# Performance work log

Measured on AMD Instinct MI355X. Metric: run time of the kernel, lower is better.

Reference implementation:

```python
import jax, jax.numpy as jnp
import numpy as np

EPS = 1e-5
ROPE_BASE = 10000.0

def rms_norm(x, w):
    return x * jax.lax.rsqrt(jnp.mean(x * x, axis=-1, keepdims=True) + EPS) * w

def rope_cos_sin(positions, head_dim):
    inv_freq = 1.0 / (ROPE_BASE ** (jnp.arange(0, head_dim, 2, dtype=jnp.float32) / head_dim))
    ang = positions.astype(jnp.float32)[:, None] * inv_freq[None, :]          # [L, hd/2]
    emb = jnp.concatenate([ang, ang], axis=-1)                                # [L, hd]
    return jnp.cos(emb), jnp.sin(emb)

def rotate_half(x):
    d = x.shape[-1] // 2
    return jnp.concatenate([-x[..., d:], x[..., :d]], axis=-1)

def apply_rope(x, cos, sin):
    # x: [B,H,L,hd]; cos/sin: [L,hd]
    return x * cos[None, None] + rotate_half(x) * sin[None, None]

def setup_inputs() -> dict:
    key = jax.random.key(0)
    ks = jax.random.split(key, 12)
    B, S, D = 1, 2048, 2048
    H, KVH, HD = 16, 8, 128
    FF, CACHE = 5632, 2048
    s = 0.02
    return {
        "hidden_states": jax.random.normal(ks[0], (B, S, D), jnp.float32),
        "k_cache": jax.random.normal(ks[1], (B, H, CACHE, HD), jnp.float32),
        "v_cache": jax.random.normal(ks[2], (B, H, CACHE, HD), jnp.float32),
        "q_w": jax.random.normal(ks[3], (H * HD, D), jnp.float32) * s,
        "k_w": jax.random.normal(ks[4], (KVH * HD, D), jnp.float32) * s,
        "v_w": jax.random.normal(ks[5], (KVH * HD, D), jnp.float32) * s,
        "o_w": jax.random.normal(ks[6], (D, H * HD), jnp.float32) * s,
        "gate_w": jax.random.normal(ks[7], (FF, D), jnp.float32) * s,
        "up_w": jax.random.normal(ks[8], (FF, D), jnp.float32) * s,
        "down_w": jax.random.normal(ks[9], (D, FF), jnp.float32) * s,
        "ln1_w": jnp.ones((D,), jnp.float32),
        "ln2_w": jnp.ones((D,), jnp.float32),
        "chunk_size": 512,
    }

def reference(hidden_states, k_cache, v_cache, q_w, k_w, v_w, o_w,
              gate_w, up_w, down_w, ln1_w, ln2_w, chunk_size):
    B, S, D = hidden_states.shape
    H = k_cache.shape[1]
    HD = k_cache.shape[-1]
    KVH = k_w.shape[0] // HD
    group = H // KVH
    prefix = k_cache.shape[2]

    # --- input RMSNorm ---
    residual = hidden_states
    h = rms_norm(hidden_states, ln1_w)

    # --- QKV projections (GQA) ---
    q = (h @ q_w.T).reshape(B, S, H, HD).transpose(0, 2, 1, 3)                # [B,H,S,hd]
    k = (h @ k_w.T).reshape(B, S, KVH, HD).transpose(0, 2, 1, 3)              # [B,KVH,S,hd]
    v = (h @ v_w.T).reshape(B, S, KVH, HD).transpose(0, 2, 1, 3)
    k = jnp.repeat(k, group, axis=1)                                          # repeat_kv -> [B,H,S,hd]
    v = jnp.repeat(v, group, axis=1)

    # --- KV-cache concat along seq ---
    keys = jnp.concatenate([k_cache, k], axis=2)                              # [B,H,P+S,hd]
    vals = jnp.concatenate([v_cache, v], axis=2)
    kv_len = prefix + S

    # --- inline RoPE: keys at 0..kv_len-1, queries at prefix..kv_len-1 ---
    cos_k, sin_k = rope_cos_sin(jnp.arange(kv_len), HD)
    q = apply_rope(q, cos_k[prefix:], sin_k[prefix:])
    keys = apply_rope(keys, cos_k, sin_k)

    # --- hybrid chunked attention mask ---
    # query i (local) sees: full cache prefix + causal positions within its own chunk
    i = jnp.arange(S)
    j = jnp.arange(kv_len)
    local_j = j - prefix
    prefix_vis = (j[None, :] < prefix)
    same_chunk = (i[:, None] // chunk_size) == (local_j[None, :] // chunk_size)
    causal = local_j[None, :] <= i[:, None]
    mask = prefix_vis | (same_chunk & causal)                                 # [S, kv_len]

    scores = jnp.einsum("bhqd,bhkd->bhqk", q, keys) / jnp.sqrt(jnp.float32(HD))
    scores = jnp.where(mask[None, None], scores, jnp.finfo(scores.dtype).min)
    probs = jax.nn.softmax(scores, axis=-1)
    attn = jnp.einsum("bhqk,bhkd->bhqd", probs, vals)                         # [B,H,S,hd]
    attn = attn.transpose(0, 2, 1, 3).reshape(B, S, H * HD) @ o_w.T

    h = residual + attn

    # --- SwiGLU MLP ---
    residual = h
    h = rms_norm(h, ln2_w)
    h = (jax.nn.silu(h @ gate_w.T) * (h @ up_w.T)) @ down_w.T
    return residual + h
```

## Files before the change

kernel.cpp:

```cpp
#include <hip/hip_runtime.h>


#define S_LEN   2048
#define D_MODEL 2048
#define NH      16
#define KVHEADS 8
#define HDIM    128
#define FFDIM   5632
#define PREFIX  2048
#define KVLEN   4096
#define SM_L2E  0.12751744f
#define MCONST  16.0f
#define LN10K_64 0.14391156831212787f

using bf16x8 = __attribute__((ext_vector_type(8))) short;
using f32x4  = __attribute__((ext_vector_type(4))) float;

__device__ __forceinline__ unsigned f2bf_u(float f) {
  unsigned u = __float_as_uint(f);
  return (u + 0x7fffu + ((u >> 16) & 1u)) >> 16;
}
__device__ __forceinline__ unsigned short f2bf(float f) { return (unsigned short)f2bf_u(f); }
__device__ __forceinline__ float bf2f(unsigned short u) {
  return __uint_as_float((unsigned)u << 16);
}
__device__ __forceinline__ unsigned pack2(float a, float b) {
  return f2bf_u(a) | (f2bf_u(b) << 16);
}
__device__ __forceinline__ uint2 pack4(float4 v) {
  uint2 r;
  r.x = pack2(v.x, v.y);
  r.y = pack2(v.z, v.w);
  return r;
}
__device__ __forceinline__ f32x4 mfma16(bf16x8 a, bf16x8 b, f32x4 c) {
  return __builtin_amdgcn_mfma_f32_16x16x32_bf16(a, b, c, 0, 0, 0);
}
__device__ __forceinline__ void gl2lds16(const unsigned short* g, unsigned short* l) {
  __builtin_amdgcn_global_load_lds(
      (__attribute__((address_space(1))) void*)(unsigned short*)g,
      (__attribute__((address_space(3))) void*)l, 16, 0, 0);
}

__device__ __forceinline__ void conv_body(const float* __restrict__ src,
                                          unsigned short* __restrict__ dst,
                                          int bseg, int tid) {
  size_t i = (size_t)bseg * 256 + tid;
  const float4* s4 = (const float4*)src;
  float4 a = s4[2 * i], b = s4[2 * i + 1];
  uint2 lo = pack4(a), hi = pack4(b);
  ((uint4*)dst)[i] = make_uint4(lo.x, lo.y, hi.x, hi.y);
}
__global__ __launch_bounds__(256) void convw_k(const float* __restrict__ src,
                                               unsigned short* __restrict__ dst) {
  conv_body(src, dst, blockIdx.x, threadIdx.x);
}
__global__ __launch_bounds__(256) void conv3_k(const float* __restrict__ q,
                                               const float* __restrict__ k,
                                               const float* __restrict__ v,
                                               unsigned short* __restrict__ dst) {
  int b = blockIdx.x;
  if (b < 2048)      conv_body(q, dst, b, threadIdx.x);
  else if (b < 3072) conv_body(k, dst + (size_t)2048 * 2048, b - 2048, threadIdx.x);
  else               conv_body(v, dst + (size_t)3072 * 2048, b - 3072, threadIdx.x);
}
__global__ __launch_bounds__(256) void conv2_k(const float* __restrict__ g,
                                               const float* __restrict__ u,
                                               unsigned short* __restrict__ wg,
                                               unsigned short* __restrict__ wu) {
  int b = blockIdx.x;
  if (b < 5632) conv_body(g, wg, b, threadIdx.x);
  else          conv_body(u, wu, b - 5632, threadIdx.x);
}

template <bool INBF>
__global__ __launch_bounds__(256) void rmsnorm_k(const void* __restrict__ xin,
                                                 const float* __restrict__ w,
                                                 unsigned short* __restrict__ out) {
  const int row = blockIdx.x, tid = threadIdx.x;
  float v[8];
  if constexpr (INBF) {
    const unsigned short* xr = (const unsigned short*)xin + (size_t)row * D_MODEL;
    uint4 u = ((const uint4*)xr)[tid];
    v[0] = bf2f((unsigned short)(u.x & 0xffff)); v[1] = bf2f((unsigned short)(u.x >> 16));
    v[2] = bf2f((unsigned short)(u.y & 0xffff)); v[3] = bf2f((unsigned short)(u.y >> 16));
    v[4] = bf2f((unsigned short)(u.z & 0xffff)); v[5] = bf2f((unsigned short)(u.z >> 16));
    v[6] = bf2f((unsigned short)(u.w & 0xffff)); v[7] = bf2f((unsigned short)(u.w >> 16));
  } else {
    const float4* xr = (const float4*)((const float*)xin + (size_t)row * D_MODEL);
    float4 a = xr[2 * tid], b = xr[2 * tid + 1];
    v[0] = a.x; v[1] = a.y; v[2] = a.z; v[3] = a.w;
    v[4] = b.x; v[5] = b.y; v[6] = b.z; v[7] = b.w;
  }
  float ss = 0.f;
#pragma unroll
  for (int i = 0; i < 8; i++) ss += v[i] * v[i];
#pragma unroll
  for (int off = 1; off < 64; off <<= 1) ss += __shfl_xor(ss, off);
  __shared__ float red[4];
  if ((tid & 63) == 0) red[tid >> 6] = ss;
  __syncthreads();
  const float sc = rsqrtf((red[0] + red[1] + red[2] + red[3]) * (1.0f / D_MODEL) + 1e-5f);
  const float4* w4 = (const float4*)w;
  float4 wa = w4[2 * tid], wb = w4[2 * tid + 1];
  float4 oa = make_float4(v[0]*sc*wa.x, v[1]*sc*wa.y, v[2]*sc*wa.z, v[3]*sc*wa.w);
  float4 ob = make_float4(v[4]*sc*wb.x, v[5]*sc*wb.y, v[6]*sc*wb.z, v[7]*sc*wb.w);
  uint2 lo = pack4(oa), hi = pack4(ob);
  ((uint4*)(out + (size_t)row * D_MODEL))[tid] = make_uint4(lo.x, lo.y, hi.x, hi.y);
}

template <int BN, int EPI>
__global__ __launch_bounds__(256) void gemm_bf(const unsigned short* __restrict__ A,
                                               const unsigned short* __restrict__ B,
                                               const void* __restrict__ res,
                                               void* __restrict__ C,
                                               int M, int N, int K) {
  constexpr int NI = BN / 32;
  __shared__ __align__(16) unsigned short lA[128 * 32];
  __shared__ __align__(16) unsigned short lB[BN * 32];
  const int tid = threadIdx.x, lane = tid & 63, wave = tid >> 6;
  const int r16 = lane & 15, q4 = lane >> 4;
  const int wm = wave >> 1, wn = wave & 1;
  const int nwg = gridDim.x * gridDim.y;
  const int flat = blockIdx.y * gridDim.x + blockIdx.x;
  const int swz = (flat & 7) * (nwg >> 3) + (flat >> 3);
  const int m0 = (swz % gridDim.x) * 128, n0 = (swz / gridDim.x) * BN;

  const int lr = lane >> 2;
  const int lc = (lane & 3) * 8;
  const unsigned short* gA0 = A + (size_t)(m0 + wave * 16 + lr) * K + lc;
  const unsigned short* gA1 = A + (size_t)(m0 + 64 + wave * 16 + lr) * K + lc;
  unsigned short* lA0 = lA + (wave * 16) * 32;
  unsigned short* lA1 = lA + (64 + wave * 16) * 32;
  const unsigned short* gB0 = B + (size_t)(n0 + wave * 16 + lr) * K + lc;
  const unsigned short* gB1 = B + (size_t)(n0 + 64 + wave * 16 + lr) * K + lc;
  unsigned short* lB0 = lB + (wave * 16) * 32;
  unsigned short* lB1 = lB + (64 + wave * 16) * 32;

  f32x4 acc[4][NI];
#pragma unroll
  for (int i = 0; i < 4; i++)
#pragma unroll
    for (int j = 0; j < NI; j++) acc[i][j] = f32x4{0.f, 0.f, 0.f, 0.f};

  for (int k0 = 0; k0 < K; k0 += 32) {
    gl2lds16(gA0, lA0);
    gl2lds16(gA1, lA1);
    gl2lds16(gB0, lB0);
    if constexpr (BN == 128) gl2lds16(gB1, lB1);
    gA0 += 32; gA1 += 32; gB0 += 32;
    if constexpr (BN == 128) gB1 += 32;
    __syncthreads();
    bf16x8 af[4], bfr[NI];
#pragma unroll
    for (int mi = 0; mi < 4; mi++)
      af[mi] = *(const bf16x8*)&lA[(wm * 64 + mi * 16 + r16) * 32 + q4 * 8];
#pragma unroll
    for (int ni = 0; ni < NI; ni++)
      bfr[ni] = *(const bf16x8*)&lB[(wn * (BN / 2) + ni * 16 + r16) * 32 + q4 * 8];
#pragma unroll
    for (int mi = 0; mi < 4; mi++)
#pragma unroll
      for (int ni = 0; ni < NI; ni++)
        acc[mi][ni] = mfma16(af[mi], bfr[ni], acc[mi][ni]);
    __syncthreads();
  }
#pragma unroll
  for (int mi = 0; mi < 4; mi++)
#pragma unroll
    for (int ni = 0; ni < NI; ni++) {
      int col = n0 + wn * (BN / 2) + ni * 16 + r16;
#pragma unroll
      for (int rr = 0; rr < 4; rr++) {
        int row = m0 + wm * 64 + mi * 16 + q4 * 4 + rr;
        size_t idx = (size_t)row * N + col;
        float v = acc[mi][ni][rr];
        if constexpr (EPI == 0) {
          ((unsigned short*)C)[idx] = f2bf(v);
        } else if constexpr (EPI == 1) {
          ((unsigned short*)C)[idx] = f2bf(v + ((const float*)res)[idx]);
        } else {
          ((float*)C)[idx] = v + bf2f(((const unsigned short*)res)[idx]);
        }
      }
    }
}

__global__ __launch_bounds__(256) void gemm_gateup(const unsigned short* __restrict__ A,
                                                   const unsigned short* __restrict__ Bg,
                                                   const unsigned short* __restrict__ Bu,
                                                   unsigned short* __restrict__ act) {
  __shared__ __align__(16) unsigned short lA[128 * 32];
  __shared__ __align__(16) unsigned short lG[64 * 32];
  __shared__ __align__(16) unsigned short lU[64 * 32];
  const int tid = threadIdx.x, lane = tid & 63, wave = tid >> 6;
  const int r16 = lane & 15, q4 = lane >> 4;
  const int wm = wave >> 1, wn = wave & 1;
  const int nwg = gridDim.x * gridDim.y;
  const int flat = blockIdx.y * gridDim.x + blockIdx.x;
  const int swz = (flat & 7) * (nwg >> 3) + (flat >> 3);
  const int m0 = (swz % gridDim.x) * 128, n0 = (swz / gridDim.x) * 64;
  const int K = D_MODEL;

  const int lr = lane >> 2, lc = (lane & 3) * 8;
  const unsigned short* gA0 = A + (size_t)(m0 + wave * 16 + lr) * K + lc;
  const unsigned short* gA1 = A + (size_t)(m0 + 64 + wave * 16 + lr) * K + lc;
  unsigned short* lA0 = lA + (wave * 16) * 32;
  unsigned short* lA1 = lA + (64 + wave * 16) * 32;
  const unsigned short* gG0 = Bg + (size_t)(n0 + wave * 16 + lr) * K + lc;
  const unsigned short* gU0 = Bu + (size_t)(n0 + wave * 16 + lr) * K + lc;
  unsigned short* lG0 = lG + (wave * 16) * 32;
  unsigned short* lU0 = lU + (wave * 16) * 32;

  f32x4 ag[4][2], au[4][2];
#pragma unroll
  for (int i = 0; i < 4; i++)
#pragma unroll
    for (int j = 0; j < 2; j++) { ag[i][j] = f32x4{0.f,0.f,0.f,0.f}; au[i][j] = f32x4{0.f,0.f,0.f,0.f}; }

  for (int k0 = 0; k0 < K; k0 += 32) {
    gl2lds16(gA0, lA0);
    gl2lds16(gA1, lA1);
    gl2lds16(gG0, lG0);
    gl2lds16(gU0, lU0);
    gA0 += 32; gA1 += 32; gG0 += 32; gU0 += 32;
    __syncthreads();
    bf16x8 af[4], bg2[2], bu2[2];
#pragma unroll
    for (int mi = 0; mi < 4; mi++)
      af[mi] = *(const bf16x8*)&lA[(wm * 64 + mi * 16 + r16) * 32 + q4 * 8];
#pragma unroll
    for (int ni = 0; ni < 2; ni++) {
      int r = (wn * 32 + ni * 16 + r16) * 32 + q4 * 8;
      bg2[ni] = *(const bf16x8*)&lG[r];
      bu2[ni] = *(const bf16x8*)&lU[r];
    }
#pragma unroll
    for (int mi = 0; mi < 4; mi++)
#pragma unroll
      for (int ni = 0; ni < 2; ni++) {
        ag[mi][ni] = mfma16(af[mi], bg2[ni], ag[mi][ni]);
        au[mi][ni] = mfma16(af[mi], bu2[ni], au[mi][ni]);
      }
    __syncthreads();
  }
#pragma unroll
  for (int mi = 0; mi < 4; mi++)
#pragma unroll
    for (int ni = 0; ni < 2; ni++) {
      int col = n0 + wn * 32 + ni * 16 + r16;
#pragma unroll
      for (int rr = 0; rr < 4; rr++) {
        int row = m0 + wm * 64 + mi * 16 + q4 * 4 + rr;
        float g = ag[mi][ni][rr], u = au[mi][ni][rr];
        float sil = g / (1.0f + __expf(-g));
        act[(size_t)row * FFDIM + col] = f2bf(sil * u);
      }
    }
}

__global__ __launch_bounds__(256) void rope_k_k(const float* __restrict__ k_cache,
                                                const unsigned short* __restrict__ qkv,
                                                unsigned short* __restrict__ keys_bf) {
  int idx = blockIdx.x * 256 + threadIdx.x;
  int d = idx & 127, j = (idx >> 7) & 4095, h = idx >> 19;
  int dd = d & 63;
  float inv = __expf(-(float)dd * LN10K_64);
  float ang = (float)j * inv;
  float c = cosf(ang), sn = sinf(ang);
  float x, xr;
  if (j < PREFIX) {
    const float* row = k_cache + ((size_t)h * PREFIX + j) * HDIM;
    x = row[d];
    xr = (d < 64) ? -row[d + 64] : row[d - 64];
  } else {
    const unsigned short* row = qkv + (size_t)(j - PREFIX) * 4096 + 2048 + (h >> 1) * HDIM;
    x = bf2f(row[d]);
    xr = (d < 64) ? -bf2f(row[d + 64]) : bf2f(row[d - 64]);
  }
  keys_bf[idx] = f2bf(x * c + xr * sn);
}

__global__ __launch_bounds__(256) void vtrans_k(const float* __restrict__ v_cache,
                                                const unsigned short* __restrict__ qkv,
                                                unsigned short* __restrict__ vals_t) {
  __shared__ float tile[32][33];
  const int h = blockIdx.z, j0 = blockIdx.x * 32, d0 = blockIdx.y * 32;
  const int t = threadIdx.x;
#pragma unroll
  for (int i = 0; i < 4; i++) {
    int e = i * 256 + t;
    int jj = e >> 5, dd = e & 31;
    float v;
    if (j0 < PREFIX)
      v = v_cache[((size_t)h * PREFIX + j0 + jj) * HDIM + d0 + dd];
    else
      v = bf2f(qkv[(size_t)(j0 - PREFIX + jj) * 4096 + 3072 + (h >> 1) * HDIM + d0 + dd]);
    tile[jj][dd] = v;
  }
  __syncthreads();
#pragma unroll
  for (int i = 0; i < 4; i++) {
    int e = i * 256 + t;
    int dd = e >> 5, jj = e & 31;
    vals_t[((size_t)h * HDIM + d0 + dd) * KVLEN + j0 + jj] = f2bf(tile[jj][dd]);
  }
}

__global__ __launch_bounds__(256) void attn_k(const unsigned short* __restrict__ qkv,
                                              const unsigned short* __restrict__ keys,
                                              const unsigned short* __restrict__ valst,
                                              const int* __restrict__ chunkp,
                                              unsigned short* __restrict__ pO,
                                              float* __restrict__ pl) {
  __shared__ __align__(16) unsigned short lK[64 * 128];
  __shared__ __align__(16) unsigned short lV[128 * 64];
  __shared__ __align__(16) unsigned short lP[4][16 * 64];
  const int flat = blockIdx.x;
  const int xcd = flat & 7, ii = flat >> 3;
  const int p = ii >> 5;
  const int seg = p >> 1;
  const int h = xcd * 2 + (p & 1);
  const int q0 = (ii & 31) * 64;
  const int tid = threadIdx.x, wave = tid >> 6, lane = tid & 63;
  const int r16 = lane & 15, q4 = lane >> 4;
  const int chunk = chunkp[0];
  const int sw = (r16 & 7) << 4;

  const int qrow = q0 + wave * 16 + r16;
  const unsigned short* qr = qkv + (size_t)qrow * 4096 + h * HDIM;
  float qx[4][8];
#pragma unroll
  for (int ks = 0; ks < 4; ks++) {
    bf16x8 raw = *(const bf16x8*)(qr + ks * 32 + q4 * 8);
#pragma unroll
    for (int j = 0; j < 8; j++) qx[ks][j] = bf2f((unsigned short)raw[j]);
  }
  const float pos = (float)(PREFIX + qrow);
  bf16x8 qf[4];
#pragma unroll
  for (int ks = 0; ks < 4; ks++)
#pragma unroll
    for (int j = 0; j < 8; j++) {
      int d = ks * 32 + q4 * 8 + j;
      float inv = __expf(-(float)(d & 63) * LN10K_64);
      float ang = pos * inv;
      float c = cosf(ang), sn = sinf(ang);
      float other = qx[ks ^ 2][j];
      float rot = (ks < 2) ? -other : other;
      qf[ks][j] = (short)f2bf(qx[ks][j] * c + rot * sn);
    }

  float lrow[4] = {0.f, 0.f, 0.f, 0.f};
  f32x4 oacc[8];
#pragma unroll
  for (int ni = 0; ni < 8; ni++) oacc[ni] = f32x4{0.f, 0.f, 0.f, 0.f};

  const int irow_base = q0 + wave * 16 + q4 * 4;
  const unsigned short* Kh = keys + (size_t)h * KVLEN * HDIM;
  const unsigned short* Vh = valst + (size_t)h * HDIM * KVLEN;

  const int krow = wave * 4 + (lane >> 4);
  const unsigned short* kSrc = Kh + (size_t)(krow * 4) * HDIM
                               + (((lane & 15) ^ (krow & 7)) * 8);
  unsigned short* kDst = lK + (wave * 4) * 128;
  const int vrow = wave * 8 + (lane >> 3);
  const unsigned short* vSrc = Vh + (size_t)vrow * KVLEN
                               + (((lane & 7) ^ ((lane >> 3) & 7)) * 8);
  unsigned short* vDst = lV + (wave * 8) * 64;

  int kt0, ktN;
  if (seg == 0)      { kt0 = 0;    ktN = 1024; }
  else if (seg == 1) { kt0 = 1024; ktN = 2048; }
  else { int cs = (q0 / chunk) * chunk; kt0 = PREFIX + cs; ktN = PREFIX + q0 + 64; }

  for (int kt = kt0; kt < ktN; kt += 64) {
    const bool domask = (seg == 2) && (kt - PREFIX + 64 > q0);
#pragma unroll
    for (int i = 0; i < 4; i++)
      gl2lds16(kSrc + (size_t)(kt + i) * HDIM, kDst + i * 16 * 128);
#pragma unroll
    for (int i = 0; i < 4; i++)
      gl2lds16(vSrc + (size_t)i * 32 * KVLEN + kt, vDst + i * 32 * 64);
    __syncthreads();
    f32x4 s[4];
#pragma unroll
    for (int j = 0; j < 4; j++) s[j] = f32x4{0.f, 0.f, 0.f, 0.f};
#pragma unroll
    for (int ks = 0; ks < 4; ks++)
#pragma unroll
      for (int j = 0; j < 4; j++) {
        bf16x8 kf = *(const bf16x8*)((const char*)lK + (j * 16 + r16) * 256
                                     + ((ks * 64 + q4 * 16) ^ sw));
        s[j] = mfma16(qf[ks], kf, s[j]);
      }
    const int klb = kt - PREFIX + r16 * 4;
#pragma unroll
    for (int rr = 0; rr < 4; rr++) {
      float e0 = fmaf(s[0][rr], SM_L2E, -MCONST);
      float e1 = fmaf(s[1][rr], SM_L2E, -MCONST);
      float e2 = fmaf(s[2][rr], SM_L2E, -MCONST);
      float e3 = fmaf(s[3][rr], SM_L2E, -MCONST);
      if (domask) {
        int irow = irow_base + rr;
        if (klb     > irow) e0 = -1e30f;
        if (klb + 1 > irow) e1 = -1e30f;
        if (klb + 2 > irow) e2 = -1e30f;
        if (klb + 3 > irow) e3 = -1e30f;
      }
      float p0 = exp2f(e0), p1 = exp2f(e1), p2 = exp2f(e2), p3 = exp2f(e3);
      lrow[rr] += (p0 + p1) + (p2 + p3);
      uint2 pk = make_uint2(pack2(p0, p1), pack2(p2, p3));
      int qrw = q4 * 4 + rr;
      *(uint2*)((char*)lP[wave] + qrw * 128 + ((r16 * 8) ^ ((qrw & 7) << 4))) = pk;
    }
    bf16x8 pf0 = *(const bf16x8*)((const char*)lP[wave] + r16 * 128
                                  + ((q4 * 16) ^ sw));
    bf16x8 pf1 = *(const bf16x8*)((const char*)lP[wave] + r16 * 128
                                  + ((64 + q4 * 16) ^ sw));
#pragma unroll
    for (int ni = 0; ni < 8; ni++) {
      bf16x8 v0 = *(const bf16x8*)((const char*)lV + (ni * 16 + r16) * 128
                                   + ((q4 * 16) ^ sw));
      oacc[ni] = mfma16(pf0, v0, oacc[ni]);
      bf16x8 v1 = *(const bf16x8*)((const char*)lV + (ni * 16 + r16) * 128
                                   + ((64 + q4 * 16) ^ sw));
      oacc[ni] = mfma16(pf1, v1, oacc[ni]);
    }
    __syncthreads();
  }

#pragma unroll
  for (int rr = 0; rr < 4; rr++) {
    lrow[rr] += __shfl_xor(lrow[rr], 1);
    lrow[rr] += __shfl_xor(lrow[rr], 2);
    lrow[rr] += __shfl_xor(lrow[rr], 4);
    lrow[rr] += __shfl_xor(lrow[rr], 8);
  }
  const size_t base = (size_t)(seg * NH + h) * S_LEN;
#pragma unroll
  for (int ni = 0; ni < 8; ni++)
#pragma unroll
    for (int rr = 0; rr < 4; rr++)
      pO[(base + irow_base + rr) * HDIM + ni * 16 + r16] = f2bf(oacc[ni][rr]);
  if (r16 == 0) {
#pragma unroll
    for (int rr = 0; rr < 4; rr++) pl[base + irow_base + rr] = lrow[rr];
  }
}

__global__ __launch_bounds__(256) void attn_combine(const unsigned short* __restrict__ pO,
                                                    const float* __restrict__ pl,
                                                    unsigned short* __restrict__ out) {
  int idx = blockIdx.x * 256 + threadIdx.x;
  int d = idx & 127, hq = idx >> 7;
  const int R = NH * S_LEN;
  float L = pl[hq] + pl[hq + R] + pl[hq + 2 * R];
  float o = bf2f(pO[(size_t)hq * HDIM + d])
          + bf2f(pO[(size_t)(hq + R) * HDIM + d])
          + bf2f(pO[(size_t)(hq + 2 * R) * HDIM + d]);
  int h = hq >> 11, q = hq & 2047;
  out[(size_t)q * D_MODEL + h * HDIM + d] = f2bf(o / L);
}

extern "C" void kernel_launch(void* const* d_in, const int* in_sizes, int n_in,
                              void* d_out, int out_size, void* d_ws, size_t ws_size,
                              hipStream_t stream) {
  (void)in_sizes; (void)n_in; (void)out_size;
  const float* hidden  = (const float*)d_in[0];
  const float* k_cache = (const float*)d_in[1];
  const float* v_cache = (const float*)d_in[2];
  const float* q_w     = (const float*)d_in[3];
  const float* k_w     = (const float*)d_in[4];
  const float* v_w     = (const float*)d_in[5];
  const float* o_w     = (const float*)d_in[6];
  const float* gate_w  = (const float*)d_in[7];
  const float* up_w    = (const float*)d_in[8];
  const float* down_w  = (const float*)d_in[9];
  const float* ln1     = (const float*)d_in[10];
  const float* ln2     = (const float*)d_in[11];
  const int*   chunkp  = (const int*)d_in[12];

  if (ws_size < 92274688) return;
  char* ws = (char*)d_ws;
  const size_t MB = 1048576;
  unsigned short* qkvpre = (unsigned short*)(ws + 0 * MB);
  unsigned short* keysbf = (unsigned short*)(ws + 16 * MB);
  unsigned short* valst  = (unsigned short*)(ws + 32 * MB);
  unsigned short* pO     = (unsigned short*)(ws + 48 * MB);
  float*          pl     = (float*)(ws + 88 * MB - 393216);
  unsigned short* WQKV   = (unsigned short*)(ws + 72 * MB);
  unsigned short* hn     = (unsigned short*)(ws + 48 * MB);
  unsigned short* attnbf = (unsigned short*)(ws + 72 * MB);
  unsigned short* WO     = (unsigned short*)(ws + 80 * MB);
  unsigned short* h2     = (unsigned short*)(ws + 48 * MB);
  unsigned short* h2n    = (unsigned short*)(ws + 56 * MB);
  unsigned short* WG     = (unsigned short*)(ws + 0 * MB);
  unsigned short* WU     = (unsigned short*)(ws + 22 * MB);
  unsigned short* act    = (unsigned short*)(ws + 64 * MB);
  unsigned short* WD     = (unsigned short*)(ws + 0 * MB);
  float* out = (float*)d_out;

  rmsnorm_k<false><<<S_LEN, 256, 0, stream>>>(hidden, ln1, hn);
  conv3_k<<<4096, 256, 0, stream>>>(q_w, k_w, v_w, WQKV);
  gemm_bf<128, 0><<<dim3(16, 32), 256, 0, stream>>>(hn, WQKV, nullptr, qkvpre,
                                                    S_LEN, 4096, D_MODEL);
  rope_k_k<<<(NH * KVLEN * HDIM) / 256, 256, 0, stream>>>(k_cache, qkvpre, keysbf);
  vtrans_k<<<dim3(KVLEN / 32, HDIM / 32, NH), 256, 0, stream>>>(v_cache, qkvpre, valst);
  attn_k<<<1536, 256, 0, stream>>>(qkvpre, keysbf, valst, chunkp, pO, pl);
  attn_combine<<<(NH * S_LEN * HDIM) / 256, 256, 0, stream>>>(pO, pl, attnbf);
  convw_k<<<2048, 256, 0, stream>>>(o_w, WO);
  gemm_bf<64, 1><<<dim3(16, 32), 256, 0, stream>>>(attnbf, WO, hidden, h2,
                                                   S_LEN, D_MODEL, D_MODEL);
  rmsnorm_k<true><<<S_LEN, 256, 0, stream>>>(h2, ln2, h2n);
  conv2_k<<<11264, 256, 0, stream>>>(gate_w, up_w, WG, WU);
  gemm_gateup<<<dim3(16, FFDIM / 64), 256, 0, stream>>>(h2n, WG, WU, act);
  convw_k<<<5632, 256, 0, stream>>>(down_w, WD);
  gemm_bf<64, 2><<<dim3(16, 32), 256, 0, stream>>>(act, WD, h2, out,
                                                   S_LEN, D_MODEL, FFDIM);
}
```

Baseline: 697.4 us.

## Enlarge gate/up GEMM N-tile and attention query tile to 128 rows

The gate/up GEMM now computes a 128x128 output tile per block instead of 128x64, so each staged A tile is reused across twice as many columns and the grid is halved. The attention kernel now gives each wave two 16-row query tiles (128 queries per block), so every K/V tile loaded into shared memory serves twice as many queries, with half the blocks. Both changes aim to cut global-to-LDS traffic per FLOP. In exchange they roughly double accumulator registers, which may lower occupancy, and the attention grid shrinks to 768 blocks. For the chunk-local segment the causal range also becomes coarser.

```diff
diff --git a/kernel.cpp b/kernel.cpp
--- a/kernel.cpp
+++ b/kernel.cpp
@@ -191,15 +191,15 @@
                                                    const unsigned short* __restrict__ Bu,
                                                    unsigned short* __restrict__ act) {
   __shared__ __align__(16) unsigned short lA[128 * 32];
-  __shared__ __align__(16) unsigned short lG[64 * 32];
-  __shared__ __align__(16) unsigned short lU[64 * 32];
+  __shared__ __align__(16) unsigned short lG[128 * 32];
+  __shared__ __align__(16) unsigned short lU[128 * 32];
   const int tid = threadIdx.x, lane = tid & 63, wave = tid >> 6;
   const int r16 = lane & 15, q4 = lane >> 4;
   const int wm = wave >> 1, wn = wave & 1;
   const int nwg = gridDim.x * gridDim.y;
   const int flat = blockIdx.y * gridDim.x + blockIdx.x;
   const int swz = (flat & 7) * (nwg >> 3) + (flat >> 3);
-  const int m0 = (swz % gridDim.x) * 128, n0 = (swz / gridDim.x) * 64;
+  const int m0 = (swz % gridDim.x) * 128, n0 = (swz / gridDim.x) * 128;
   const int K = D_MODEL;
 
   const int lr = lane >> 2, lc = (lane & 3) * 8;
@@ -208,37 +208,43 @@
   unsigned short* lA0 = lA + (wave * 16) * 32;
   unsigned short* lA1 = lA + (64 + wave * 16) * 32;
   const unsigned short* gG0 = Bg + (size_t)(n0 + wave * 16 + lr) * K + lc;
+  const unsigned short* gG1 = Bg + (size_t)(n0 + 64 + wave * 16 + lr) * K + lc;
   const unsigned short* gU0 = Bu + (size_t)(n0 + wave * 16 + lr) * K + lc;
+  const unsigned short* gU1 = Bu + (size_t)(n0 + 64 + wave * 16 + lr) * K + lc;
   unsigned short* lG0 = lG + (wave * 16) * 32;
+  unsigned short* lG1 = lG + (64 + wave * 16) * 32;
   unsigned short* lU0 = lU + (wave * 16) * 32;
-
-  f32x4 ag[4][2], au[4][2];
+  unsigned short* lU1 = lU + (64 + wave * 16) * 32;
+
+  f32x4 ag[4][4], au[4][4];
 #pragma unroll
   for (int i = 0; i < 4; i++)
 #pragma unroll
-    for (int j = 0; j < 2; j++) { ag[i][j] = f32x4{0.f,0.f,0.f,0.f}; au[i][j] = f32x4{0.f,0.f,0.f,0.f}; }
+    for (int j = 0; j < 4; j++) { ag[i][j] = f32x4{0.f,0.f,0.f,0.f}; au[i][j] = f32x4{0.f,0.f,0.f,0.f}; }
 
   for (int k0 = 0; k0 < K; k0 += 32) {
     gl2lds16(gA0, lA0);
     gl2lds16(gA1, lA1);
     gl2lds16(gG0, lG0);
+    gl2lds16(gG1, lG1);
     gl2lds16(gU0, lU0);
-    gA0 += 32; gA1 += 32; gG0 += 32; gU0 += 32;
+    gl2lds16(gU1, lU1);
+    gA0 += 32; gA1 += 32; gG0 += 32; gG1 += 32; gU0 += 32; gU1 += 32;
     __syncthreads();
-    bf16x8 af[4], bg2[2], bu2[2];
+    bf16x8 af[4], bg2[4], bu2[4];
 #pragma unroll
     for (int mi = 0; mi < 4; mi++)
       af[mi] = *(const bf16x8*)&lA[(wm * 64 + mi * 16 + r16) * 32 + q4 * 8];
 #pragma unroll
-    for (int ni = 0; ni < 2; ni++) {
-      int r = (wn * 32 + ni * 16 + r16) * 32 + q4 * 8;
+    for (int ni = 0; ni < 4; ni++) {
+      int r = (wn * 64 + ni * 16 + r16) * 32 + q4 * 8;
       bg2[ni] = *(const bf16x8*)&lG[r];
       bu2[ni] = *(const bf16x8*)&lU[r];
     }
 #pragma unroll
     for (int mi = 0; mi < 4; mi++)
 #pragma unroll
-      for (int ni = 0; ni < 2; ni++) {
+      for (int ni = 0; ni < 4; ni++) {
         ag[mi][ni] = mfma16(af[mi], bg2[ni], ag[mi][ni]);
         au[mi][ni] = mfma16(af[mi], bu2[ni], au[mi][ni]);
       }
@@ -247,8 +253,8 @@
 #pragma unroll
   for (int mi = 0; mi < 4; mi++)
 #pragma unroll
-    for (int ni = 0; ni < 2; ni++) {
-      int col = n0 + wn * 32 + ni * 16 + r16;
+    for (int ni = 0; ni < 4; ni++) {
+      int col = n0 + wn * 64 + ni * 16 + r16;
 #pragma unroll
       for (int rr = 0; rr < 4; rr++) {
         int row = m0 + wm * 64 + mi * 16 + q4 * 4 + rr;
@@ -315,48 +321,57 @@
                                               float* __restrict__ pl) {
   __shared__ __align__(16) unsigned short lK[64 * 128];
   __shared__ __align__(16) unsigned short lV[128 * 64];
-  __shared__ __align__(16) unsigned short lP[4][16 * 64];
+  __shared__ __align__(16) unsigned short lP[4][2][16 * 64];
   const int flat = blockIdx.x;
   const int xcd = flat & 7, ii = flat >> 3;
-  const int p = ii >> 5;
+  const int p = ii >> 4;
   const int seg = p >> 1;
   const int h = xcd * 2 + (p & 1);
-  const int q0 = (ii & 31) * 64;
+  const int q0 = (ii & 15) * 128;
   const int tid = threadIdx.x, wave = tid >> 6, lane = tid & 63;
   const int r16 = lane & 15, q4 = lane >> 4;
   const int chunk = chunkp[0];
   const int sw = (r16 & 7) << 4;
 
-  const int qrow = q0 + wave * 16 + r16;
-  const unsigned short* qr = qkv + (size_t)qrow * 4096 + h * HDIM;
-  float qx[4][8];
-#pragma unroll
-  for (int ks = 0; ks < 4; ks++) {
-    bf16x8 raw = *(const bf16x8*)(qr + ks * 32 + q4 * 8);
-#pragma unroll
-    for (int j = 0; j < 8; j++) qx[ks][j] = bf2f((unsigned short)raw[j]);
-  }
-  const float pos = (float)(PREFIX + qrow);
-  bf16x8 qf[4];
-#pragma unroll
-  for (int ks = 0; ks < 4; ks++)
-#pragma unroll
-    for (int j = 0; j < 8; j++) {
-      int d = ks * 32 + q4 * 8 + j;
-      float inv = __expf(-(float)(d & 63) * LN10K_64);
-      float ang = pos * inv;
-      float c = cosf(ang), sn = sinf(ang);
-      float other = qx[ks ^ 2][j];
-      float rot = (ks < 2) ? -other : other;
-      qf[ks][j] = (short)f2bf(qx[ks][j] * c + rot * sn);
-    }
-
-  float lrow[4] = {0.f, 0.f, 0.f, 0.f};
-  f32x4 oacc[8];
-#pragma unroll
-  for (int ni = 0; ni < 8; ni++) oacc[ni] = f32x4{0.f, 0.f, 0.f, 0.f};
-
-  const int irow_base = q0 + wave * 16 + q4 * 4;
+  bf16x8 qf[2][4];
+#pragma unroll
+  for (int qt = 0; qt < 2; qt++) {
+    const int qrow = q0 + wave * 32 + qt * 16 + r16;
+    const unsigned short* qr = qkv + (size_t)qrow * 4096 + h * HDIM;
+    float qx[4][8];
+#pragma unroll
+    for (int ks = 0; ks < 4; ks++) {
+      bf16x8 raw = *(const bf16x8*)(qr + ks * 32 + q4 * 8);
+#pragma unroll
+      for (int j = 0; j < 8; j++) qx[ks][j] = bf2f((unsigned short)raw[j]);
+    }
+    const float pos = (float)(PREFIX + qrow);
+#pragma unroll
+    for (int ks = 0; ks < 4; ks++)
+#pragma unroll
+      for (int j = 0; j < 8; j++) {
+        int d = ks * 32 + q4 * 8 + j;
+        float inv = __expf(-(float)(d & 63) * LN10K_64);
+        float ang = pos * inv;
+        float c = cosf(ang), sn = sinf(ang);
+        float other = qx[ks ^ 2][j];
+        float rot = (ks < 2) ? -other : other;
+        qf[qt][ks][j] = (short)f2bf(qx[ks][j] * c + rot * sn);
+      }
+  }
+
+  float lrow[2][4];
+#pragma unroll
+  for (int qt = 0; qt < 2; qt++)
+#pragma unroll
+    for (int rr = 0; rr < 4; rr++) lrow[qt][rr] = 0.f;
+  f32x4 oacc[2][8];
+#pragma unroll
+  for (int qt = 0; qt < 2; qt++)
+#pragma unroll
+    for (int ni = 0; ni < 8; ni++) oacc[qt][ni] = f32x4{0.f, 0.f, 0.f, 0.f};
+
+  const int irow0 = q0 + wave * 32 + q4 * 4;
   const unsigned short* Kh = keys + (size_t)h * KVLEN * HDIM;
   const unsigned short* Vh = valst + (size_t)h * HDIM * KVLEN;
 
@@ -372,7 +387,7 @@
   int kt0, ktN;
   if (seg == 0)      { kt0 = 0;    ktN = 1024; }
   else if (seg == 1) { kt0 = 1024; ktN = 2048; }
-  else { int cs = (q0 / chunk) * chunk; kt0 = PREFIX + cs; ktN = PREFIX + q0 + 64; }
+  else { int cs = (q0 / chunk) * chunk; kt0 = PREFIX + cs; ktN = PREFIX + q0 + 128; }
 
   for (int kt = kt0; kt < ktN; kt += 64) {
     const bool domask = (seg == 2) && (kt - PREFIX + 64 > q0);
@@ -383,69 +398,86 @@
     for (int i = 0; i < 4; i++)
       gl2lds16(vSrc + (size_t)i * 32 * KVLEN + kt, vDst + i * 32 * 64);
     __syncthreads();
-    f32x4 s[4];
-#pragma unroll
-    for (int j = 0; j < 4; j++) s[j] = f32x4{0.f, 0.f, 0.f, 0.f};
+    f32x4 s[2][4];
+#pragma unroll
+    for (int qt = 0; qt < 2; qt++)
+#pragma unroll
+      for (int j = 0; j < 4; j++) s[qt][j] = f32x4{0.f, 0.f, 0.f, 0.f};
 #pragma unroll
     for (int ks = 0; ks < 4; ks++)
 #pragma unroll
       for (int j = 0; j < 4; j++) {
         bf16x8 kf = *(const bf16x8*)((const char*)lK + (j * 16 + r16) * 256
                                      + ((ks * 64 + q4 * 16) ^ sw));
-        s[j] = mfma16(qf[ks], kf, s[j]);
+        s[0][j] = mfma16(qf[0][ks], kf, s[0][j]);
+        s[1][j] = mfma16(qf[1][ks], kf, s[1][j]);
       }
     const int klb = kt - PREFIX + r16 * 4;
 #pragma unroll
-    for (int rr = 0; rr < 4; rr++) {
-      float e0 = fmaf(s[0][rr], SM_L2E, -MCONST);
-      float e1 = fmaf(s[1][rr], SM_L2E, -MCONST);
-      float e2 = fmaf(s[2][rr], SM_L2E, -MCONST);
-      float e3 = fmaf(s[3][rr], SM_L2E, -MCONST);
-      if (domask) {
-        int irow = irow_base + rr;
-        if (klb     > irow) e0 = -1e30f;
-        if (klb + 1 > irow) e1 = -1e30f;
-        if (klb + 2 > irow) e2 = -1e30f;
-        if (klb + 3 > irow) e3 = -1e30f;
+    for (int qt = 0; qt < 2; qt++)
+#pragma unroll
+      for (int rr = 0; rr < 4; rr++) {
+        float e0 = fmaf(s[qt][0][rr], SM_L2E, -MCONST);
+        float e1 = fmaf(s[qt][1][rr], SM_L2E, -MCONST);
+        float e2 = fmaf(s[qt][2][rr], SM_L2E, -MCONST);
+        float e3 = fmaf(s[qt][3][rr], SM_L2E, -MCONST);
+        if (domask) {
+          int irow = irow0 + qt * 16 + rr;
+          if (klb     > irow) e0 = -1e30f;
+          if (klb + 1 > irow) e1 = -1e30f;
+          if (klb + 2 > irow) e2 = -1e30f;
+          if (klb + 3 > irow) e3 = -1e30f;
+        }
+        float p0 = exp2f(e0), p1 = exp2f(e1), p2 = exp2f(e2), p3 = exp2f(e3);
+        lrow[qt][rr] += (p0 + p1) + (p2 + p3);
+        uint2 pk = make_uint2(pack2(p0, p1), pack2(p2, p3));
+        int qrw = q4 * 4 + rr;
+        *(uint2*)((char*)lP[wave][qt] + qrw * 128 + ((r16 * 8) ^ ((qrw & 7) << 4))) = pk;
       }
-      float p0 = exp2f(e0), p1 = exp2f(e1), p2 = exp2f(e2), p3 = exp2f(e3);
-      lrow[rr] += (p0 + p1) + (p2 + p3);
-      uint2 pk = make_uint2(pack2(p0, p1), pack2(p2, p3));
-      int qrw = q4 * 4 + rr;
-      *(uint2*)((char*)lP[wave] + qrw * 128 + ((r16 * 8) ^ ((qrw & 7) << 4))) = pk;
-    }
-    bf16x8 pf0 = *(const bf16x8*)((const char*)lP[wave] + r16 * 128
-                                  + ((q4 * 16) ^ sw));
-    bf16x8 pf1 = *(const bf16x8*)((const char*)lP[wave] + r16 * 128
-                                  + ((64 + q4 * 16) ^ sw));
+    bf16x8 pf0[2], pf1[2];
+#pragma unroll
+    for (int qt = 0; qt < 2; qt++) {
+      pf0[qt] = *(const bf16x8*)((const char*)lP[wave][qt] + r16 * 128
+                                 + ((q4 * 16) ^ sw));
+      pf1[qt] = *(const bf16x8*)((const char*)lP[wave][qt] + r16 * 128
+                                 + ((64 + q4 * 16) ^ sw));
+    }
 #pragma unroll
     for (int ni = 0; ni < 8; ni++) {
       bf16x8 v0 = *(const bf16x8*)((const char*)lV + (ni * 16 + r16) * 128
                                    + ((q4 * 16) ^ sw));
-      oacc[ni] = mfma16(pf0, v0, oacc[ni]);
+      oacc[0][ni] = mfma16(pf0[0], v0, oacc[0][ni]);
+      oacc[1][ni] = mfma16(pf0[1], v0, oacc[1][ni]);
       bf16x8 v1 = *(const bf16x8*)((const char*)lV + (ni * 16 + r16) * 128
                                    + ((64 + q4 * 16) ^ sw));
-      oacc[ni] = mfma16(pf1, v1, oacc[ni]);
+      oacc[0][ni] = mfma16(pf1[0], v1, oacc[0][ni]);
+      oacc[1][ni] = mfma16(pf1[1], v1, oacc[1][ni]);
     }
     __syncthreads();
   }
 
 #pragma unroll
-  for (int rr = 0; rr < 4; rr++) {
-    lrow[rr] += __shfl_xor(lrow[rr], 1);
-    lrow[rr] += __shfl_xor(lrow[rr], 2);
-    lrow[rr] += __shfl_xor(lrow[rr], 4);
-    lrow[rr] += __shfl_xor(lrow[rr], 8);
-  }
+  for (int qt = 0; qt < 2; qt++)
+#pragma unroll
+    for (int rr = 0; rr < 4; rr++) {
+      lrow[qt][rr] += __shfl_xor(lrow[qt][rr], 1);
+      lrow[qt][rr] += __shfl_xor(lrow[qt][rr], 2);
+      lrow[qt][rr] += __shfl_xor(lrow[qt][rr], 4);
+      lrow[qt][rr] += __shfl_xor(lrow[qt][rr], 8);
+    }
   const size_t base = (size_t)(seg * NH + h) * S_LEN;
 #pragma unroll
-  for (int ni = 0; ni < 8; ni++)
-#pragma unroll
-    for (int rr = 0; rr < 4; rr++)
-      pO[(base + irow_base + rr) * HDIM + ni * 16 + r16] = f2bf(oacc[ni][rr]);
-  if (r16 == 0) {
-#pragma unroll
-    for (int rr = 0; rr < 4; rr++) pl[base + irow_base + rr] = lrow[rr];
+  for (int qt = 0; qt < 2; qt++) {
+    const int irow_t = irow0 + qt * 16;
+#pragma unroll
+    for (int ni = 0; ni < 8; ni++)
+#pragma unroll
+      for (int rr = 0; rr < 4; rr++)
+        pO[(base + irow_t + rr) * HDIM + ni * 16 + r16] = f2bf(oacc[qt][ni][rr]);
+    if (r16 == 0) {
+#pragma unroll
+      for (int rr = 0; rr < 4; rr++) pl[base + irow_t + rr] = lrow[qt][rr];
+    }
   }
 }
 
@@ -507,14 +539,14 @@
                                                     S_LEN, 4096, D_MODEL);
   rope_k_k<<<(NH * KVLEN * HDIM) / 256, 256, 0, stream>>>(k_cache, qkvpre, keysbf);
   vtrans_k<<<dim3(KVLEN / 32, HDIM / 32, NH), 256, 0, stream>>>(v_cache, qkvpre, valst);
-  attn_k<<<1536, 256, 0, stream>>>(qkvpre, keysbf, valst, chunkp, pO, pl);
+  attn_k<<<768, 256, 0, stream>>>(qkvpre, keysbf, valst, chunkp, pO, pl);
   attn_combine<<<(NH * S_LEN * HDIM) / 256, 256, 0, stream>>>(pO, pl, attnbf);
   convw_k<<<2048, 256, 0, stream>>>(o_w, WO);
   gemm_bf<64, 1><<<dim3(16, 32), 256, 0, stream>>>(attnbf, WO, hidden, h2,
                                                    S_LEN, D_MODEL, D_MODEL);
   rmsnorm_k<true><<<S_LEN, 256, 0, stream>>>(h2, ln2, h2n);
   conv2_k<<<11264, 256, 0, stream>>>(gate_w, up_w, WG, WU);
-  gemm_gateup<<<dim3(16, FFDIM / 64), 256, 0, stream>>>(h2n, WG, WU, act);
+  gemm_gateup<<<dim3(16, FFDIM / 128), 256, 0, stream>>>(h2n, WG, WU, act);
   convw_k<<<5632, 256, 0, stream>>>(down_w, WD);
   gemm_bf<64, 2><<<dim3(16, 32), 256, 0, stream>>>(act, WD, h2, out,
                                                    S_LEN, D_MODEL, FFDIM);
```

Measured after the change: 814.7 us. +16.8%, slower.
